# Kernel optimization log

Hardware: AMD Instinct MI355X
Metric: run time of the kernel (lower is better)

Reference implementation:

```python
import jax, jax.numpy as jnp
import numpy as np


def setup_inputs() -> dict:
    key = jax.random.key(0)
    k1, k2 = jax.random.split(key)
    B, D, H, W = 32, 64, 32, 32
    K = 1024
    z_e = jax.random.normal(k1, (B, D, H, W), dtype=jnp.float32)
    # original init: uniform(-1/K, 1/K); use same scale
    emb = jax.random.uniform(k2, (K, D), dtype=jnp.float32, minval=-1.0 / K, maxval=1.0 / K)
    return {"z_e": z_e, "emb": emb}


COMMITMENT_COST = 0.25


def reference(z_e, emb):
    # z_e: [B, D, H, W], emb: [K, D]
    B, D, H, W = z_e.shape
    K = emb.shape[0]
    z = jnp.transpose(z_e, (0, 2, 3, 1))           # [B, H, W, D]
    flat = z.reshape(-1, D)                        # [N, D]
    N = flat.shape[0]

    dist = (
        jnp.sum(flat * flat, axis=1, keepdims=True)
        + jnp.sum(emb * emb, axis=1)
        - 2.0 * flat @ emb.T
    )
    idx = jnp.argmin(dist, axis=1)                 # [N]
    encodings = jax.nn.one_hot(idx, K, dtype=flat.dtype)  # [N, K]
    z_q = (encodings @ emb).reshape(z.shape)       # [B, H, W, D]

    e_latent_loss = jnp.mean((jax.lax.stop_gradient(z_q) - z) ** 2)
    q_latent_loss = jnp.mean((z_q - jax.lax.stop_gradient(z)) ** 2)
    loss = q_latent_loss + COMMITMENT_COST * e_latent_loss

    # straight-through estimator
    z_st = z + jax.lax.stop_gradient(z_q - z)

    avg_probs = jnp.sum(encodings, axis=0) / jnp.float32(N)
    perplexity = jnp.exp(-jnp.sum(avg_probs * jnp.log(avg_probs + 1e-10)))

    return (jnp.transpose(z_st, (0, 3, 1, 2)), loss, perplexity, encodings)
```

## Files before the change

kernel.cpp:

```cpp
#include <hip/hip_runtime.h>
#include <stdint.h>
#include <math.h>

constexpr int Nn  = 32768;
constexpr int Kk  = 1024;

constexpr int OUT0_N   = 32 * 64 * 1024;
constexpr int OUT_LOSS = OUT0_N;
constexpr int OUT_PERP = OUT0_N + 1;
constexpr int OUT_ENC  = OUT0_N + 2;

constexpr size_t WS_CNT = 0;
constexpr size_t WS_LP  = 4096;
constexpr size_t WS_KEY = 69632;

__device__ __forceinline__ float norm64v(const float4* __restrict__ p) {
#pragma clang fp contract(off)
    float tt[64];
#pragma unroll
    for (int q = 0; q < 16; ++q) {
        float4 v = p[q];
        tt[4 * q + 0] = v.x * v.x;
        tt[4 * q + 1] = v.y * v.y;
        tt[4 * q + 2] = v.z * v.z;
        tt[4 * q + 3] = v.w * v.w;
    }
    float r[8];
#pragma unroll
    for (int j = 0; j < 8; ++j) r[j] = tt[j];
#pragma unroll
    for (int i = 8; i < 64; i += 8)
#pragma unroll
        for (int j = 0; j < 8; ++j) r[j] += tt[i + j];
    return ((r[0] + r[1]) + (r[2] + r[3])) + ((r[4] + r[5]) + (r[6] + r[7]));
}

__device__ __forceinline__ uint32_t fsort(float f) {
    uint32_t b = __float_as_uint(f);
    return (b & 0x80000000u) ? ~b : (b | 0x80000000u);
}

__global__ __launch_bounds__(256, 2)
void dist_kernel(const float* __restrict__ z_e, const float* __restrict__ emb,
                 unsigned long long* __restrict__ minkey) {
    __shared__ float xs[128 * 68];
    __shared__ float es[128 * 68];
    __shared__ float An_s[128];
    __shared__ float Bn_s[128];
    const int tid = threadIdx.x;
    const int rg = blockIdx.x >> 3, cg = blockIdx.x & 7;
    const int n0 = rg * 128;
    const int b = n0 >> 10, hw0 = n0 & 1023;
    const float* zb = z_e + (size_t)b * 65536 + hw0;

    {
        int hwi = tid & 127;
        int d4g = tid >> 7;
#pragma unroll
        for (int it = 0; it < 8; ++it) {
            int dbase = (d4g + it * 2) * 4;
            float4 v;
            v.x = zb[(size_t)(dbase + 0) * 1024 + hwi];
            v.y = zb[(size_t)(dbase + 1) * 1024 + hwi];
            v.z = zb[(size_t)(dbase + 2) * 1024 + hwi];
            v.w = zb[(size_t)(dbase + 3) * 1024 + hwi];
            *(float4*)&xs[hwi * 68 + dbase] = v;
        }
    }
    {
        const float4* ep = (const float4*)(emb + (size_t)cg * 128 * 64);
#pragma unroll
        for (int it = 0; it < 8; ++it) {
            int j = tid + it * 256;
            float4 v = ep[j];
            int c = j >> 4, d4 = j & 15;
            *(float4*)&es[c * 68 + d4 * 4] = v;
        }
    }
    __syncthreads();

    if (tid < 128) {
        An_s[tid] = norm64v((const float4*)&xs[tid * 68]);
    } else {
        int c = tid - 128;
        Bn_s[c] = norm64v((const float4*)&es[c * 68]);
    }
    __syncthreads();

    const int tx = tid & 15, ty = tid >> 4;
    float acc[8][8];
#pragma unroll
    for (int i = 0; i < 8; ++i)
#pragma unroll
        for (int j = 0; j < 8; ++j) acc[i][j] = 0.0f;

#pragma unroll 1
    for (int d4 = 0; d4 < 16; ++d4) {
        float4 xv[8], ev[8];
#pragma unroll
        for (int i = 0; i < 8; ++i) xv[i] = *(const float4*)&xs[(ty + 16 * i) * 68 + d4 * 4];
#pragma unroll
        for (int j = 0; j < 8; ++j) ev[j] = *(const float4*)&es[(tx + 16 * j) * 68 + d4 * 4];
#pragma unroll
        for (int i = 0; i < 8; ++i)
#pragma unroll
            for (int j = 0; j < 8; ++j) {
                float a = acc[i][j];
                a = __builtin_fmaf(xv[i].x, ev[j].x, a);
                a = __builtin_fmaf(xv[i].y, ev[j].y, a);
                a = __builtin_fmaf(xv[i].z, ev[j].z, a);
                a = __builtin_fmaf(xv[i].w, ev[j].w, a);
                acc[i][j] = a;
            }
    }

    float Ar[8], Bc[8];
#pragma unroll
    for (int i = 0; i < 8; ++i) Ar[i] = An_s[ty + 16 * i];
#pragma unroll
    for (int j = 0; j < 8; ++j) Bc[j] = Bn_s[tx + 16 * j];

#pragma unroll
    for (int i = 0; i < 8; ++i) {
        unsigned long long best = ~0ULL;
#pragma unroll
        for (int j = 0; j < 8; ++j) {
            float s = Ar[i] + Bc[j];
            float dist = s - 2.0f * acc[i][j];
            unsigned long long key = ((unsigned long long)fsort(dist) << 32)
                                   | (unsigned)(cg * 128 + tx + 16 * j);
            best = (key < best) ? key : best;
        }
#pragma unroll
        for (int m = 1; m < 16; m <<= 1) {
            unsigned long long o = __shfl_xor(best, m, 64);
            best = (o < best) ? o : best;
        }
        if (tx == 0) atomicMin(&minkey[n0 + ty + 16 * i], best);
    }
}

__global__ void finish_kernel(const float* __restrict__ z_e,
                              const float* __restrict__ emb,
                              const unsigned long long* __restrict__ minkey,
                              uint32_t* __restrict__ counts,
                              double* __restrict__ lp,
                              float* __restrict__ out) {
    __shared__ uint32_t scode[4];
    __shared__ double lred[4];
    const int t = threadIdx.x;
    const int r4 = blockIdx.x * 4;
    if (t < 4) {
        uint32_t code = (uint32_t)minkey[r4 + t];
        scode[t] = code;
        atomicAdd(&counts[code], 1u);
    }
    __syncthreads();

    {
        const int b = r4 >> 10, hw = (r4 & 1023) + (t & 3);
        const int d = t >> 2;
        const size_t off = (size_t)b * 65536 + (size_t)d * 1024 + hw;
        float z  = z_e[off];
        float zq = emb[(size_t)scode[t & 3] * 64 + d];
        float tt = zq - z;
        out[off] = z + tt;
        double ls = (double)tt * (double)tt;
#pragma unroll
        for (int m = 32; m >= 1; m >>= 1) ls += __shfl_down(ls, m, 64);
        if ((t & 63) == 0) lred[t >> 6] = ls;
    }
    __syncthreads();
    if (t == 0) lp[blockIdx.x] = lred[0] + lred[1] + lred[2] + lred[3];

    float* enc = out + OUT_ENC;
#pragma unroll
    for (int i = 0; i < 4; ++i) {
        uint32_t code = scode[i];
        uint32_t c0 = (uint32_t)(t * 4);
        float4 v;
        v.x = (code == c0 + 0u) ? 1.0f : 0.0f;
        v.y = (code == c0 + 1u) ? 1.0f : 0.0f;
        v.z = (code == c0 + 2u) ? 1.0f : 0.0f;
        v.w = (code == c0 + 3u) ? 1.0f : 0.0f;
        ((float4*)enc)[(size_t)(r4 + i) * 256 + t] = v;
    }
}

__global__ void scalar_kernel(const uint32_t* __restrict__ counts,
                              const double* __restrict__ lp,
                              float* __restrict__ out) {
    __shared__ double redl[4], redh[4];
    const int t = threadIdx.x;
    double ls = 0.0;
    for (int i = t; i < 8192; i += 256) ls += lp[i];
    double h = 0.0;
    for (int i = t; i < Kk; i += 256) {
        double p = (double)counts[i] * (1.0 / 32768.0);
        h += p * log(p + 1e-10);
    }
#pragma unroll
    for (int m = 32; m >= 1; m >>= 1) { ls += __shfl_down(ls, m, 64); h += __shfl_down(h, m, 64); }
    if ((t & 63) == 0) { redl[t >> 6] = ls; redh[t >> 6] = h; }
    __syncthreads();
    if (t == 0) {
        double L = redl[0] + redl[1] + redl[2] + redl[3];
        double H = redh[0] + redh[1] + redh[2] + redh[3];
        out[OUT_PERP] = (float)exp(-H);
        float m32 = (float)(L * (1.0 / 2097152.0));
        out[OUT_LOSS] = m32 + 0.25f * m32;
    }
}

extern "C" void kernel_launch(void* const* d_in, const int* in_sizes, int n_in,
                              void* d_out, int out_size, void* d_ws, size_t ws_size,
                              hipStream_t stream) {
    const float* z_e = (const float*)d_in[0];
    const float* emb = (const float*)d_in[1];
    float* out = (float*)d_out;
    char* ws = (char*)d_ws;

    uint32_t* counts = (uint32_t*)(ws + WS_CNT);
    double*   lp     = (double*)(ws + WS_LP);
    unsigned long long* minkey = (unsigned long long*)(ws + WS_KEY);

    hipMemsetAsync(ws + WS_CNT, 0, 4096, stream);
    hipMemsetAsync(ws + WS_KEY, 0xFF, (size_t)Nn * 8, stream);

    dist_kernel<<<2048, 256, 0, stream>>>(z_e, emb, minkey);
    finish_kernel<<<8192, 256, 0, stream>>>(z_e, emb, minkey, counts, lp, out);
    scalar_kernel<<<1, 256, 0, stream>>>(counts, lp, out);
}
```

Baseline: 236.9 us.

## Zero one-hot output in dist kernel and scatter ones in a coarser finish kernel

```diff
diff --git a/kernel.cpp b/kernel.cpp
--- a/kernel.cpp
+++ b/kernel.cpp
@@ -42,7 +42,9 @@
 
 __global__ __launch_bounds__(256, 2)
 void dist_kernel(const float* __restrict__ z_e, const float* __restrict__ emb,
-                 unsigned long long* __restrict__ minkey) {
+                 unsigned long long* __restrict__ minkey,
+                 uint32_t* __restrict__ counts,
+                 float* __restrict__ out) {
     __shared__ float xs[128 * 68];
     __shared__ float es[128 * 68];
     __shared__ float An_s[128];
@@ -77,6 +79,9 @@
             *(float4*)&es[c * 68 + d4 * 4] = v;
         }
     }
+    if (blockIdx.x == 0) {
+        ((uint4*)counts)[tid] = make_uint4(0u, 0u, 0u, 0u);
+    }
     __syncthreads();
 
     if (tid < 128) {
@@ -86,6 +91,13 @@
         Bn_s[c] = norm64v((const float4*)&es[c * 68]);
     }
     __syncthreads();
+
+    {
+        float4 z4 = make_float4(0.0f, 0.0f, 0.0f, 0.0f);
+        float4* encz = (float4*)(out + OUT_ENC) + (size_t)blockIdx.x * 4096;
+#pragma unroll
+        for (int it = 0; it < 16; ++it) encz[it * 256 + tid] = z4;
+    }
 
     const int tx = tid & 15, ty = tid >> 4;
     float acc[8][8];
@@ -140,51 +152,60 @@
     }
 }
 
-__global__ void finish_kernel(const float* __restrict__ z_e,
-                              const float* __restrict__ emb,
-                              const unsigned long long* __restrict__ minkey,
-                              uint32_t* __restrict__ counts,
-                              double* __restrict__ lp,
-                              float* __restrict__ out) {
-    __shared__ uint32_t scode[4];
+__global__ __launch_bounds__(256)
+void finish_kernel(const float* __restrict__ z_e,
+                   const float* __restrict__ emb,
+                   const unsigned long long* __restrict__ minkey,
+                   uint32_t* __restrict__ counts,
+                   double* __restrict__ lp,
+                   float* __restrict__ out) {
+    __shared__ uint32_t scode[64];
     __shared__ double lred[4];
     const int t = threadIdx.x;
-    const int r4 = blockIdx.x * 4;
-    if (t < 4) {
-        uint32_t code = (uint32_t)minkey[r4 + t];
+    const int n0 = blockIdx.x * 64;
+    const int b = n0 >> 10, hw0 = n0 & 1023;
+
+    if (t < 64) {
+        uint32_t code = (uint32_t)minkey[n0 + t];
         scode[t] = code;
         atomicAdd(&counts[code], 1u);
-    }
-    __syncthreads();
-
-    {
-        const int b = r4 >> 10, hw = (r4 & 1023) + (t & 3);
-        const int d = t >> 2;
-        const size_t off = (size_t)b * 65536 + (size_t)d * 1024 + hw;
-        float z  = z_e[off];
-        float zq = emb[(size_t)scode[t & 3] * 64 + d];
-        float tt = zq - z;
-        out[off] = z + tt;
-        double ls = (double)tt * (double)tt;
-#pragma unroll
-        for (int m = 32; m >= 1; m >>= 1) ls += __shfl_down(ls, m, 64);
-        if ((t & 63) == 0) lred[t >> 6] = ls;
-    }
+        out[(size_t)OUT_ENC + (size_t)(n0 + t) * 1024 + code] = 1.0f;
+    }
+    __syncthreads();
+
+    const int hwi = t & 63, dg = t >> 6;
+    const uint32_t code = scode[hwi];
+    const float4* er4 = (const float4*)(emb + (size_t)code * 64) + dg * 4;
+    const size_t base = (size_t)b * 65536 + (size_t)(dg * 16) * 1024 + hw0 + hwi;
+
+    double ls = 0.0;
+#pragma unroll
+    for (int k4 = 0; k4 < 4; ++k4) {
+        float4 e4 = er4[k4];
+        float f0 = e4.x, f1 = e4.y, f2 = e4.z, f3 = e4.w;
+        size_t off = base + (size_t)(k4 * 4) * 1024;
+        {
+            float z = z_e[off];            float tt = f0 - z;
+            out[off] = z + tt;             ls += (double)tt * (double)tt;
+        }
+        {
+            float z = z_e[off + 1024];     float tt = f1 - z;
+            out[off + 1024] = z + tt;      ls += (double)tt * (double)tt;
+        }
+        {
+            float z = z_e[off + 2048];     float tt = f2 - z;
+            out[off + 2048] = z + tt;      ls += (double)tt * (double)tt;
+        }
+        {
+            float z = z_e[off + 3072];     float tt = f3 - z;
+            out[off + 3072] = z + tt;      ls += (double)tt * (double)tt;
+        }
+    }
+#pragma unroll
+    for (int m = 32; m >= 1; m >>= 1) ls += __shfl_down(ls, m, 64);
+    if ((t & 63) == 0) lred[t >> 6] = ls;
     __syncthreads();
     if (t == 0) lp[blockIdx.x] = lred[0] + lred[1] + lred[2] + lred[3];
-
-    float* enc = out + OUT_ENC;
-#pragma unroll
-    for (int i = 0; i < 4; ++i) {
-        uint32_t code = scode[i];
-        uint32_t c0 = (uint32_t)(t * 4);
-        float4 v;
-        v.x = (code == c0 + 0u) ? 1.0f : 0.0f;
-        v.y = (code == c0 + 1u) ? 1.0f : 0.0f;
-        v.z = (code == c0 + 2u) ? 1.0f : 0.0f;
-        v.w = (code == c0 + 3u) ? 1.0f : 0.0f;
-        ((float4*)enc)[(size_t)(r4 + i) * 256 + t] = v;
-    }
 }
 
 __global__ void scalar_kernel(const uint32_t* __restrict__ counts,
@@ -193,7 +214,7 @@
     __shared__ double redl[4], redh[4];
     const int t = threadIdx.x;
     double ls = 0.0;
-    for (int i = t; i < 8192; i += 256) ls += lp[i];
+    for (int i = t; i < 512; i += 256) ls += lp[i];
     double h = 0.0;
     for (int i = t; i < Kk; i += 256) {
         double p = (double)counts[i] * (1.0 / 32768.0);
@@ -224,10 +245,9 @@
     double*   lp     = (double*)(ws + WS_LP);
     unsigned long long* minkey = (unsigned long long*)(ws + WS_KEY);
 
-    hipMemsetAsync(ws + WS_CNT, 0, 4096, stream);
     hipMemsetAsync(ws + WS_KEY, 0xFF, (size_t)Nn * 8, stream);
 
-    dist_kernel<<<2048, 256, 0, stream>>>(z_e, emb, minkey);
-    finish_kernel<<<8192, 256, 0, stream>>>(z_e, emb, minkey, counts, lp, out);
+    dist_kernel<<<2048, 256, 0, stream>>>(z_e, emb, minkey, counts, out);
+    finish_kernel<<<512, 256, 0, stream>>>(z_e, emb, minkey, counts, lp, out);
     scalar_kernel<<<1, 256, 0, stream>>>(counts, lp, out);
 }
```

New measurement: 214.7 us. 9.4% less time.
